# Performance work log

Measured on AMD Instinct MI355X. Metric: run time of the kernel, lower is better.

Reference implementation:

```python
import jax, jax.numpy as jnp
import numpy as np

B, S, V, E, H, NL, DFF = 16, 16, 64, 64, 8, 4, 2048
L = S * V
DH = E // H
NUM_GRIDS = 100
POI_DIM = 8
OV_DIM = 8


def setup_inputs() -> dict:
    key = jax.random.key(0)
    ks = jax.random.split(key, 32)
    sc = 0.05
    inp = {}
    inp['features'] = jax.random.normal(ks[0], (B, S, V, 3), jnp.float32)
    inp['overlap_tag'] = jax.random.randint(ks[1], (B, S, V), 0, 3)
    inp['poi_id'] = jax.random.randint(ks[2], (B, S, V), 0, NUM_GRIDS + 1)
    # embedders
    inp['W_raw'] = jax.random.normal(ks[3], (3, E), jnp.float32) * sc
    inp['b_raw'] = jnp.zeros((E,), jnp.float32)
    inp['pos_tab'] = jax.random.normal(ks[4], (S, E), jnp.float32) * sc
    inp['type_tab'] = jax.random.normal(ks[5], (V, E), jnp.float32) * sc
    inp['poi_tab'] = jax.random.normal(ks[6], (NUM_GRIDS + 1, POI_DIM), jnp.float32) * sc
    inp['overlap_tab'] = jax.random.normal(ks[7], (3, OV_DIM), jnp.float32) * sc
    inp['W_comb'] = jax.random.normal(ks[8], (E + OV_DIM + POI_DIM, E), jnp.float32) * sc
    inp['b_comb'] = jnp.zeros((E,), jnp.float32)
    # transformer layers (stacked over NL)
    inp['Wqkv'] = jax.random.normal(ks[9], (NL, E, 3 * E), jnp.float32) * sc
    inp['bqkv'] = jnp.zeros((NL, 3 * E), jnp.float32)
    inp['Wo'] = jax.random.normal(ks[10], (NL, E, E), jnp.float32) * sc
    inp['bo'] = jnp.zeros((NL, E), jnp.float32)
    inp['ln1_s'] = jnp.ones((NL, E), jnp.float32)
    inp['ln1_b'] = jnp.zeros((NL, E), jnp.float32)
    inp['W1'] = jax.random.normal(ks[11], (NL, E, DFF), jnp.float32) * sc
    inp['b1'] = jnp.zeros((NL, DFF), jnp.float32)
    inp['W2'] = jax.random.normal(ks[12], (NL, DFF, E), jnp.float32) * sc
    inp['b2'] = jnp.zeros((NL, E), jnp.float32)
    inp['ln2_s'] = jnp.ones((NL, E), jnp.float32)
    inp['ln2_b'] = jnp.zeros((NL, E), jnp.float32)
    inp['W_head'] = jax.random.normal(ks[13], (E, 3), jnp.float32) * sc
    inp['b_head'] = jnp.zeros((3,), jnp.float32)
    return inp


def _layer_norm(x, s, b):
    m = x.mean(-1, keepdims=True)
    v = ((x - m) ** 2).mean(-1, keepdims=True)
    return (x - m) / jnp.sqrt(v + 1e-5) * s + b


def _forward(features, overlap_tag, poi_id, W_raw, b_raw, pos_tab, type_tab,
             poi_tab, overlap_tab, W_comb, b_comb, Wqkv, bqkv, Wo, bo,
             ln1_s, ln1_b, W1, b1, W2, b2, ln2_s, ln2_b, W_head, b_head):
    # padding_idx=0 rows are zero (as in nn.Embedding(padding_idx=0))
    poi_tab = poi_tab.at[0].set(0.0)
    overlap_tab = overlap_tab.at[0].set(0.0)

    zero_mask = (features.sum(-1) == 0).reshape(B, L)  # [B, L]
    ov_idx = jnp.maximum(overlap_tag, 0)
    poi_idx = jnp.maximum(poi_id, 0)

    feat_e = features @ W_raw + b_raw                    # [B,S,V,E]
    concat = jnp.concatenate([feat_e, overlap_tab[ov_idx], poi_tab[poi_idx]], axis=-1)
    x = (concat @ W_comb + b_comb).reshape(B, L, E)      # [B,L,E]

    t_idx = jnp.repeat(jnp.arange(S), V)                 # [L]
    v_idx = jnp.tile(jnp.arange(V), S)                   # [L]
    struct_mask = (t_idx[:, None] != t_idx[None, :]) & (v_idx[:, None] != v_idx[None, :])
    full_mask = struct_mask[None] | zero_mask[:, None, :] | zero_mask[:, :, None]  # [B,L,L]
    bias = jnp.where(full_mask, -jnp.inf, 0.0)[:, None, :, :]  # [B,1,L,L]

    x = x + pos_tab[t_idx][None] + type_tab[v_idx][None]

    scale = 1.0 / jnp.sqrt(jnp.asarray(DH, x.dtype))
    for l in range(NL):
        qkv = x @ Wqkv[l] + bqkv[l]                      # [B,L,3E]
        q, k, v = jnp.split(qkv, 3, axis=-1)
        q = q.reshape(B, L, H, DH)
        k = k.reshape(B, L, H, DH)
        v = v.reshape(B, L, H, DH)
        scores = jnp.einsum('bqhd,bkhd->bhqk', q, k) * scale + bias
        attn = jax.nn.softmax(scores, axis=-1)
        o = jnp.einsum('bhqk,bkhd->bqhd', attn, v).reshape(B, L, E)
        x = _layer_norm(x + o @ Wo[l] + bo[l], ln1_s[l], ln1_b[l])
        ff = jax.nn.relu(x @ W1[l] + b1[l]) @ W2[l] + b2[l]
        x = _layer_norm(x + ff, ln2_s[l], ln2_b[l])

    last = x.reshape(B, S, V, E)[:, -1]                  # [B,V,E]
    return last @ W_head + b_head                        # [B,V,3]


def reference(features, overlap_tag, poi_id, W_raw, b_raw, pos_tab, type_tab,
              poi_tab, overlap_tab, W_comb, b_comb, Wqkv, bqkv, Wo, bo,
              ln1_s, ln1_b, W1, b1, W2, b2, ln2_s, ln2_b, W_head, b_head):
    return _forward(features, overlap_tag, poi_id, W_raw, b_raw, pos_tab, type_tab,
                    poi_tab, overlap_tab, W_comb, b_comb, Wqkv, bqkv, Wo, bo,
                    ln1_s, ln1_b, W1, b1, W2, b2, ln2_s, ln2_b, W_head, b_head)
```

## Files before the change

kernel.cpp:

```cpp
#include <hip/hip_runtime.h>
#include <math.h>

#define BB 16
#define SS 16
#define VVV 64
#define EE 64
#define HHH 8
#define NLAYER 4
#define DFF_ 2048
#define LL 1024
#define BL 16384
#define PERL 131072

typedef __attribute__((ext_vector_type(8))) _Float16 half8;
typedef __attribute__((ext_vector_type(4))) _Float16 half4v;
typedef __attribute__((ext_vector_type(2))) _Float16 half2v;
typedef __attribute__((ext_vector_type(4))) float f32x4;

#if defined(__has_builtin)
#if __has_builtin(__builtin_amdgcn_fdot2)
#define HAVE_FDOT2 1
#endif
#endif

#define SW64(m, k)  (((m) << 6) + ((((k) >> 3) ^ ((m) & 7)) << 3) + ((k) & 7))


__global__ __launch_bounds__(256) void k_prep(
    const float* __restrict__ W1, const float* __restrict__ W2,
    const float* __restrict__ Wqkv, const float* __restrict__ Wo,
    const float* __restrict__ Wcomb,
    _Float16* __restrict__ w1f, _Float16* __restrict__ w2f,
    _Float16* __restrict__ wqkvf, _Float16* __restrict__ wof,
    _Float16* __restrict__ wcombt)
{
  __shared__ float t[64 * 65];
  int bx = blockIdx.x;
  int cc = threadIdx.x & 63, rr = threadIdx.x >> 6;

  if (bx >= 272) {
    int r0 = (bx - 272) * 64;
#pragma unroll
    for (int i = 0; i < 16; i++) {
      int r = i * 4 + rr;
      if (r0 + r < 80) t[r * 65 + cc] = Wcomb[(size_t)(r0 + r) * 64 + cc];
    }
    __syncthreads();
#pragma unroll
    for (int i = 0; i < 16; i++) {
      int c = i * 4 + rr;
      if (r0 + c < 80) wcombt[(size_t)cc * 80 + r0 + c] = (_Float16)t[c * 65 + cc];
    }
    return;
  }

  const float* src; _Float16* dst; int astr;
  if (bx < 128) {
    int l = bx >> 5, g = bx & 31;
    src = W1 + (size_t)l * PERL + g * 64; astr = 2048;
    dst = w1f + (size_t)(l * 32 + g) * 4096;
  } else if (bx < 256) {
    int j = bx - 128; int l = j >> 5, g = j & 31;
    src = W2 + (size_t)l * PERL + (size_t)g * 64 * 64; astr = 64;
    dst = w2f + (size_t)(l * 32 + g) * 4096;
  } else if (bx < 268) {
    int j = bx - 256; int l = j / 3, g = j % 3;
    src = Wqkv + (size_t)l * 64 * 192 + g * 64; astr = 192;
    dst = wqkvf + (size_t)(l * 3 + g) * 4096;
  } else {
    int l = bx - 268;
    src = Wo + (size_t)l * 4096; astr = 64;
    dst = wof + (size_t)l * 4096;
  }
#pragma unroll
  for (int i = 0; i < 16; i++) {
    int a = i * 4 + rr;
    t[cc * 65 + a] = src[(size_t)a * astr + cc];
  }
  __syncthreads();
#pragma unroll
  for (int it = 0; it < 2; it++) {
    int c = threadIdx.x + it * 256;
    int frag = c >> 6, lane = c & 63;
    int m = (frag >> 1) * 16 + (lane & 15);
    int k0 = (frag & 1) * 32 + (lane >> 4) * 8;
    const float* tr = &t[m * 65 + k0];
    half8 h;
#pragma unroll
    for (int j = 0; j < 8; j++) h[j] = (_Float16)tr[j];
    *(half8*)&dst[(size_t)c * 8] = h;
  }
}

__device__ __forceinline__ void qkv_nb(
    const half8 (&af)[2][2], const _Float16* __restrict__ wqkvf,
    const float* __restrict__ bqkv, _Float16* __restrict__ qbuf,
    _Float16* __restrict__ kbuf, _Float16* __restrict__ vbuf,
    int bx, int nb, int wm, int wn, int lane)
{
  int quad = lane >> 4, l15 = lane & 15;
  const _Float16* bt = wqkvf + (size_t)nb * 4096;
  half8 bf[2][2];
#pragma unroll
  for (int nt = 0; nt < 2; nt++)
#pragma unroll
    for (int ks = 0; ks < 2; ks++)
      bf[nt][ks] = *(const half8*)&bt[(size_t)(((wn * 2 + nt) * 2 + ks) * 512) +
                                      lane * 8];
  f32x4 acc[2][2];
#pragma unroll
  for (int mt = 0; mt < 2; mt++)
#pragma unroll
    for (int nt = 0; nt < 2; nt++) {
      float bv = bqkv[nb * 64 + wn * 32 + nt * 16 + l15];
      acc[mt][nt] = (f32x4){bv, bv, bv, bv};
    }
#pragma unroll
  for (int ks = 0; ks < 2; ks++)
#pragma unroll
    for (int mt = 0; mt < 2; mt++)
#pragma unroll
      for (int nt = 0; nt < 2; nt++)
        acc[mt][nt] = __builtin_amdgcn_mfma_f32_16x16x32_f16(
            af[mt][ks], bf[nt][ks], acc[mt][nt], 0, 0, 0);
  _Float16* dst = (nb == 0) ? qbuf : ((nb == 1) ? kbuf : vbuf);
#pragma unroll
  for (int mt = 0; mt < 2; mt++)
#pragma unroll
    for (int nt = 0; nt < 2; nt++) {
      int col = wn * 32 + nt * 16 + l15;
      int h = col >> 3, d = col & 7;
#pragma unroll
      for (int r = 0; r < 4; r++) {
        int row = bx * 64 + wm * 32 + mt * 16 + quad * 4 + r;
        int b = row >> 10, rb = row & 1023;
        dst[((size_t)(b * 8 + h) * 1024 + rb) * 8 + d] = (_Float16)acc[mt][nt][r];
      }
    }
}

__device__ __forceinline__ void ffn_load2(
    const _Float16* __restrict__ w1f, const _Float16* __restrict__ w2f, int g,
    half8 (&a1)[2][2], half8 (&b2w)[2][2], int wn, int lane)
{
  const _Float16* w1t_ = w1f + (size_t)g * 4096;
  const _Float16* w2t_ = w2f + (size_t)g * 4096;
#pragma unroll
  for (int ht = 0; ht < 2; ht++)
#pragma unroll
    for (int ks = 0; ks < 2; ks++)
      a1[ht][ks] = *(const half8*)&w1t_[(size_t)(((wn * 2 + ht) * 2 + ks) * 512) +
                                        lane * 8];
#pragma unroll
  for (int nt = 0; nt < 2; nt++)
#pragma unroll
    for (int ks = 0; ks < 2; ks++)
      b2w[nt][ks] = *(const half8*)&w2t_[(size_t)(((wn * 2 + nt) * 2 + ks) * 512) +
                                         lane * 8];
}

__device__ __forceinline__ void ffn_step2(
    const half8 (&a1)[2][2], const half8 (&b2w)[2][2], const half8 (&xb)[2][2],
    _Float16* hsbuf, const float* __restrict__ b1, int g, f32x4 (&acc)[2][2],
    int wn, int lane)
{
  int quad = lane >> 4, l15 = lane & 15;
  f32x4 hacc[2][2];
#pragma unroll
  for (int ht = 0; ht < 2; ht++)
#pragma unroll
    for (int mt = 0; mt < 2; mt++) hacc[ht][mt] = (f32x4){0.f, 0.f, 0.f, 0.f};
#pragma unroll
  for (int ks = 0; ks < 2; ks++)
#pragma unroll
    for (int ht = 0; ht < 2; ht++)
#pragma unroll
      for (int mt = 0; mt < 2; mt++)
        hacc[ht][mt] = __builtin_amdgcn_mfma_f32_16x16x32_f16(
            a1[ht][ks], xb[mt][ks], hacc[ht][mt], 0, 0, 0);
#pragma unroll
  for (int ht = 0; ht < 2; ht++) {
    float4 bb = *(const float4*)&b1[g * 64 + wn * 32 + ht * 16 + quad * 4];
#pragma unroll
    for (int mt = 0; mt < 2; mt++) {
      f32x4 hv = hacc[ht][mt];
      half4v hp = (half4v){
          (_Float16)fmaxf(hv[0] + bb.x, 0.f), (_Float16)fmaxf(hv[1] + bb.y, 0.f),
          (_Float16)fmaxf(hv[2] + bb.z, 0.f), (_Float16)fmaxf(hv[3] + bb.w, 0.f)};
      *(half4v*)&hsbuf[SW64(mt * 16 + l15, wn * 32 + ht * 16 + quad * 4)] = hp;
    }
  }
  __syncthreads();
#pragma unroll
  for (int ks = 0; ks < 2; ks++)
#pragma unroll
    for (int mt = 0; mt < 2; mt++) {
      half8 a2 = *(const half8*)&hsbuf[SW64(mt * 16 + l15, ks * 32 + quad * 8)];
#pragma unroll
      for (int nt = 0; nt < 2; nt++)
        acc[mt][nt] = __builtin_amdgcn_mfma_f32_16x16x32_f16(a2, b2w[nt][ks],
                                                             acc[mt][nt], 0, 0, 0);
    }
}

__global__ __launch_bounds__(256) void k_embqkv(
    const float* __restrict__ features, const int* __restrict__ ovtag,
    const int* __restrict__ poiid, const float* __restrict__ W_raw,
    const float* __restrict__ b_raw, const float* __restrict__ ov_tab,
    const float* __restrict__ poi_tab, const _Float16* __restrict__ wcombt,
    const float* __restrict__ b_comb, const float* __restrict__ pos_tab,
    const float* __restrict__ type_tab, float* __restrict__ x1,
    float* __restrict__ zm, const _Float16* __restrict__ wqkvf,
    const float* __restrict__ bqkv, _Float16* __restrict__ qbuf,
    _Float16* __restrict__ kbuf, _Float16* __restrict__ vbuf)
{
  constexpr int KP = 104;
  __shared__ _Float16 As[64 * KP];
  __shared__ _Float16 Bs[64 * KP];
  __shared__ _Float16 xs[4096];
  int tid = threadIdx.x;
  int raw = blockIdx.x;
  int bx = ((raw & 7) << 5) + (raw >> 3);
  int m0 = bx * 64;
  int wave = tid >> 6, lane = tid & 63, quad = lane >> 4, l15 = lane & 15;
  int wm = wave >> 1, wn = wave & 1;
  for (int p = tid; p < 1536; p += 256) {
    int r = p / 24, s = p - r * 24; int c = s * 4;
    int row = m0 + r;
    float f0 = features[row * 3 + 0];
    float f1 = features[row * 3 + 1];
    float f2 = features[row * 3 + 2];
    if (s == 0) zm[row] = ((f0 + f1 + f2) == 0.f) ? 1.f : 0.f;
    half4v h;
#pragma unroll
    for (int j = 0; j < 4; j++) {
      int cc = c + j; float v;
      if (cc < 64) {
        v = b_raw[cc] + f0 * W_raw[cc] + f1 * W_raw[64 + cc] + f2 * W_raw[128 + cc];
      } else if (cc < 72) {
        int tt = ovtag[row]; v = (tt <= 0) ? 0.f : ov_tab[tt * 8 + cc - 64];
      } else if (cc < 80) {
        int tt = poiid[row]; v = (tt <= 0) ? 0.f : poi_tab[tt * 8 + cc - 72];
      } else v = 0.f;
      h[j] = (_Float16)v;
    }
    *(half4v*)&As[r * KP + c] = h;
  }
  for (int p = tid; p < 1536; p += 256) {
    int r = p / 24, s = p - r * 24; int c = s * 4;
    half4v h = (half4v){0, 0, 0, 0};
    if (c < 80) h = *(const half4v*)&wcombt[r * 80 + c];
    *(half4v*)&Bs[r * KP + c] = h;
  }
  __syncthreads();
  f32x4 acc[2][2];
#pragma unroll
  for (int mt = 0; mt < 2; mt++)
#pragma unroll
    for (int nt = 0; nt < 2; nt++) {
      float bv = b_comb[wn * 32 + nt * 16 + l15];
      acc[mt][nt] = (f32x4){bv, bv, bv, bv};
    }
#pragma unroll
  for (int ks = 0; ks < 3; ks++) {
    half8 af[2], bf[2];
#pragma unroll
    for (int mt = 0; mt < 2; mt++)
      af[mt] = *(const half8*)&As[(wm * 32 + mt * 16 + l15) * KP + ks * 32 + quad * 8];
#pragma unroll
    for (int nt = 0; nt < 2; nt++)
      bf[nt] = *(const half8*)&Bs[(wn * 32 + nt * 16 + l15) * KP + ks * 32 + quad * 8];
#pragma unroll
    for (int mt = 0; mt < 2; mt++)
#pragma unroll
      for (int nt = 0; nt < 2; nt++)
        acc[mt][nt] = __builtin_amdgcn_mfma_f32_16x16x32_f16(af[mt], bf[nt],
                                                             acc[mt][nt], 0, 0, 0);
  }
#pragma unroll
  for (int mt = 0; mt < 2; mt++)
#pragma unroll
    for (int nt = 0; nt < 2; nt++)
#pragma unroll
      for (int r = 0; r < 4; r++) {
        int lrow = wm * 32 + mt * 16 + quad * 4 + r;
        int row = m0 + lrow;
        int col = wn * 32 + nt * 16 + l15;
        int l = row & (LL - 1);
        float v = acc[mt][nt][r] +
            pos_tab[(l >> 6) * 64 + col] + type_tab[(l & 63) * 64 + col];
        x1[(size_t)row * 64 + col] = v;
        xs[SW64(lrow, col)] = (_Float16)v;
      }
  __syncthreads();
  half8 af[2][2];
#pragma unroll
  for (int mt = 0; mt < 2; mt++)
#pragma unroll
    for (int ks = 0; ks < 2; ks++)
      af[mt][ks] = *(const half8*)&xs[SW64(wm * 32 + mt * 16 + l15,
                                           ks * 32 + quad * 8)];
  for (int nb = 0; nb < 3; nb++)
    qkv_nb(af, wqkvf, bqkv, qbuf, kbuf, vbuf, bx, nb, wm, wn, lane);
}

__global__ __launch_bounds__(256, 2) void k_layerf(
    const _Float16* __restrict__ qin, const _Float16* __restrict__ kin,
    const _Float16* __restrict__ vin, const float* __restrict__ zm,
    const _Float16* __restrict__ wof, const float* __restrict__ bo,
    float* __restrict__ x1,
    const float* __restrict__ ln1_s, const float* __restrict__ ln1_b,
    const _Float16* __restrict__ w1f, const _Float16* __restrict__ w2f,
    const float* __restrict__ b1, const float* __restrict__ b2,
    const float* __restrict__ ln2_s, const float* __restrict__ ln2_b,
    const _Float16* __restrict__ wqkvf, const float* __restrict__ bqkv,
    _Float16* __restrict__ qout, _Float16* __restrict__ kout,
    _Float16* __restrict__ vout, int doqkv,
    const float* __restrict__ Wh, const float* __restrict__ bh,
    float* __restrict__ out)
{
  __shared__ float ots[32 * 68];
  __shared__ __align__(16) _Float16 xs[2048];
  __shared__ float x2f[2048];
  __shared__ __align__(16) _Float16 hs[4][2048];
  __shared__ __align__(16) _Float16 os[2048];
  __shared__ float zsh[1024];
  __shared__ __align__(16) _Float16 kvs[8192];
  __shared__ float ots2[32 * 68];
  int tid = threadIdx.x;
  int raw = blockIdx.x;
  int bx = ((raw & 7) << 6) + (raw >> 3);
  int r0 = bx * 32;
  int rb0 = r0 & 1023;
  int wave = tid >> 6, lane = tid & 63;
  int quad = lane >> 4, l15 = lane & 15;
  int grp = wave >> 1, wn = wave & 1;
  int b = r0 >> 10;
  int tq0 = rb0 >> 6;

  for (int p = tid; p < 1024; p += 256)
    zsh[p] = (zm[b * LL + p] != 0.f) ? -20000.f : 0.f;
  for (int p = tid; p < 512; p += 256) {
    int h = p >> 6, row = p & 63;
    size_t gidx = ((size_t)(b * 8 + h) * 1024 + tq0 * 64 + row) * 8;
    *(half8*)&kvs[h * 512 + row * 8] = *(const half8*)&kin[gidx];
    *(half8*)&kvs[4096 + h * 512 + row * 8] = *(const half8*)&vin[gidx];
  }

  half8 obf[2][2];
#pragma unroll
  for (int nt = 0; nt < 2; nt++)
#pragma unroll
    for (int ks = 0; ks < 2; ks++)
      obf[nt][ks] = *(const half8*)&wof[(size_t)(((wn * 2 + nt) * 2 + ks) * 512) +
                                        lane * 8];
  float x1pre[8];
#pragma unroll
  for (int i = 0; i < 8; i++)
    x1pre[i] = x1[(size_t)(r0 + wave * 8 + i) * 64 + lane];
  float ln1sv = ln1_s[lane], ln1bv = ln1_b[lane];
  float ln2sv = ln2_s[lane], ln2bv = ln2_b[lane];
  float fb2 = b2[lane];
  __syncthreads();

  {
    int lr = tid & 31, hh = tid >> 5;
    int rb = rb0 + lr;
    int vq = rb & 63;
    const _Float16* kb = kin + (size_t)(b * 8 + hh) * 8192;
    const _Float16* vb = vin + (size_t)(b * 8 + hh) * 8192;
    half8 qh = *(const half8*)&qin[(size_t)(b * 8 + hh) * 8192 + (size_t)rb * 8];
    const float scale = 0.3535533905932738f;
    float m = -10000.f, lsum = 0.f;
    float acc[8] = {0.f, 0.f, 0.f, 0.f, 0.f, 0.f, 0.f, 0.f};
    bool zmq = (zsh[rb] < -1.f);

    auto dot = [&](half8 kk) -> float {
      float s = 0.f;
#ifdef HAVE_FDOT2
#pragma unroll
      for (int j = 0; j < 4; j++) {
        half2v qa = (half2v){qh[2 * j], qh[2 * j + 1]};
        half2v ka = (half2v){kk[2 * j], kk[2 * j + 1]};
        s = __builtin_amdgcn_fdot2(qa, ka, s, false);
      }
#else
#pragma unroll
      for (int j = 0; j < 8; j++) s += (float)qh[j] * (float)kk[j];
#endif
      return s;
    };
    auto update = [&](float s, half8 vv) {
      float nm = fmaxf(m, s);
      float r = __expf(m - nm);
      float p = __expf(s - nm);
      lsum = lsum * r + p;
#pragma unroll
      for (int d = 0; d < 8; d++) acc[d] = acc[d] * r + p * (float)vv[d];
      m = nm;
    };

    if (!zmq) {
      for (int base = 0; base < 64; base += 4) {
        half8 kk[4], vv[4]; float sv[4];
#pragma unroll
        for (int j = 0; j < 4; j++) {
          kk[j] = *(const half8*)&kvs[hh * 512 + (base + j) * 8];
          vv[j] = *(const half8*)&kvs[4096 + hh * 512 + (base + j) * 8];
        }
#pragma unroll
        for (int j = 0; j < 4; j++)
          sv[j] = dot(kk[j]) * scale + zsh[tq0 * 64 + base + j];
#pragma unroll
        for (int j = 0; j < 4; j++) update(sv[j], vv[j]);
      }
      for (int bb = 0; bb < 5; bb++) {
        half8 kk[3], vv[3]; float sv[3];
#pragma unroll
        for (int j = 0; j < 3; j++) {
          int cc = bb * 3 + j;
          int tt = cc + ((cc >= tq0) ? 1 : 0);
          int k = tt * 64 + vq;
          kk[j] = *(const half8*)&kb[(size_t)k * 8];
          vv[j] = *(const half8*)&vb[(size_t)k * 8];
          sv[j] = zsh[k];
        }
#pragma unroll
        for (int j = 0; j < 3; j++) sv[j] += dot(kk[j]) * scale;
#pragma unroll
        for (int j = 0; j < 3; j++) update(sv[j], vv[j]);
      }
    }
    float inv = (lsum > 0.f) ? 1.f / lsum : 0.f;
    half8 o;
#pragma unroll
    for (int d = 0; d < 8; d++) o[d] = (_Float16)(acc[d] * inv);
    *(half8*)&os[SW64(lr, hh * 8)] = o;
  }
  __syncthreads();

  {
    half8 af[2];
#pragma unroll
    for (int ks = 0; ks < 2; ks++)
      af[ks] = *(const half8*)&os[SW64(grp * 16 + l15, ks * 32 + quad * 8)];
    f32x4 acc[2];
#pragma unroll
    for (int nt = 0; nt < 2; nt++) {
      float bv = bo[wn * 32 + nt * 16 + l15];
      acc[nt] = (f32x4){bv, bv, bv, bv};
    }
#pragma unroll
    for (int ks = 0; ks < 2; ks++)
#pragma unroll
      for (int nt = 0; nt < 2; nt++)
        acc[nt] = __builtin_amdgcn_mfma_f32_16x16x32_f16(af[ks], obf[nt][ks],
                                                         acc[nt], 0, 0, 0);
#pragma unroll
    for (int nt = 0; nt < 2; nt++)
#pragma unroll
      for (int r = 0; r < 4; r++)
        ots[(grp * 16 + quad * 4 + r) * 68 + wn * 32 + nt * 16 + l15] = acc[nt][r];
  }
  half8 a1x[2][2], b2x[2][2], a1y[2][2], b2y[2][2];
  ffn_load2(w1f, w2f, grp, a1x, b2x, wn, lane);
  __syncthreads();
  for (int i = 0; i < 8; i++) {
    int row = wave * 8 + i;
    float val = ots[row * 68 + lane] + x1pre[i];
    float sum = val;
#pragma unroll
    for (int o = 32; o > 0; o >>= 1) sum += __shfl_xor(sum, o);
    float mean = sum * (1.f / 64.f);
    float d = val - mean;
    float sq = d * d;
#pragma unroll
    for (int o = 32; o > 0; o >>= 1) sq += __shfl_xor(sq, o);
    float xv = d * rsqrtf(sq * (1.f / 64.f) + 1e-5f) * ln1sv + ln1bv;
    x2f[row * 64 + lane] = xv;
    xs[SW64(row, lane)] = (_Float16)xv;
  }
  __syncthreads();

  half8 xb[2][2];
#pragma unroll
  for (int mt = 0; mt < 2; mt++)
#pragma unroll
    for (int ks = 0; ks < 2; ks++)
      xb[mt][ks] = *(const half8*)&xs[SW64(mt * 16 + l15, ks * 32 + quad * 8)];
  f32x4 acc[2][2];
#pragma unroll
  for (int mt = 0; mt < 2; mt++)
#pragma unroll
    for (int nt = 0; nt < 2; nt++) {
      float bv = (grp == 0) ? b2[wn * 32 + nt * 16 + l15] : 0.f;
      acc[mt][nt] = (f32x4){bv, bv, bv, bv};
    }
  for (int ii = 0; ii < 8; ii++) {
    ffn_load2(w1f, w2f, ii * 4 + 2 + grp, a1y, b2y, wn, lane);
    ffn_step2(a1x, b2x, xb, &hs[grp][0], b1, ii * 4 + grp, acc, wn, lane);
    if (ii < 7) ffn_load2(w1f, w2f, ii * 4 + 4 + grp, a1x, b2x, wn, lane);
    ffn_step2(a1y, b2y, xb, &hs[grp + 2][0], b1, ii * 4 + 2 + grp, acc, wn, lane);
  }
  __syncthreads();
  if (grp == 0) {
#pragma unroll
    for (int mt = 0; mt < 2; mt++)
#pragma unroll
      for (int nt = 0; nt < 2; nt++)
#pragma unroll
        for (int r = 0; r < 4; r++)
          ots[(mt * 16 + quad * 4 + r) * 68 + wn * 32 + nt * 16 + l15] =
              acc[mt][nt][r];
  }
  __syncthreads();
  if (grp == 1) {
#pragma unroll
    for (int mt = 0; mt < 2; mt++)
#pragma unroll
      for (int nt = 0; nt < 2; nt++)
#pragma unroll
        for (int r = 0; r < 4; r++)
          ots[(mt * 16 + quad * 4 + r) * 68 + wn * 32 + nt * 16 + l15] +=
              acc[mt][nt][r];
  }
  __syncthreads();
  for (int i = 0; i < 8; i++) {
    int row = wave * 8 + i;
    size_t off = (size_t)(r0 + row) * 64 + lane;
    float val = ots[row * 68 + lane] + x2f[row * 64 + lane];
    float sum = val;
#pragma unroll
    for (int o = 32; o > 0; o >>= 1) sum += __shfl_xor(sum, o);
    float mean = sum * (1.f / 64.f);
    float d = val - mean;
    float sq = d * d;
#pragma unroll
    for (int o = 32; o > 0; o >>= 1) sq += __shfl_xor(sq, o);
    float xv = d * rsqrtf(sq * (1.f / 64.f) + 1e-5f) * ln2sv + ln2bv;
    x1[off] = xv;
    x2f[row * 64 + lane] = xv;
    xs[SW64(row, lane)] = (_Float16)xv;
  }
  if (!doqkv) {
    __syncthreads();
    if ((bx & 31) >= 30 && tid < 96) {
      int bb2 = bx >> 5;
      int i = tid / 3, j = tid - i * 3;
      int vglob = (bx & 1) * 32 + i;
      float a = bh[j];
      for (int e = 0; e < 64; e++)
        a += x2f[i * 64 + e] * Wh[e * 3 + j];
      out[((size_t)(bb2 * 64 + vglob)) * 3 + j] = a;
    }
    return;
  }
  __syncthreads();
  half8 af[2][2];
#pragma unroll
  for (int mt = 0; mt < 2; mt++)
#pragma unroll
    for (int ks = 0; ks < 2; ks++)
      af[mt][ks] = *(const half8*)&xs[SW64(mt * 16 + l15, ks * 32 + quad * 8)];
  for (int nb = 0; nb < 3; nb++) {
    const _Float16* bt = wqkvf + (size_t)nb * 4096;
    half8 bf[2];
#pragma unroll
    for (int ks = 0; ks < 2; ks++)
      bf[ks] = *(const half8*)&bt[(size_t)((wave * 2 + ks) * 512) + lane * 8];
    f32x4 qacc[2];
#pragma unroll
    for (int mt = 0; mt < 2; mt++) {
      float bv = bqkv[nb * 64 + wave * 16 + l15];
      qacc[mt] = (f32x4){bv, bv, bv, bv};
    }
#pragma unroll
    for (int ks = 0; ks < 2; ks++)
#pragma unroll
      for (int mt = 0; mt < 2; mt++)
        qacc[mt] = __builtin_amdgcn_mfma_f32_16x16x32_f16(af[mt][ks], bf[ks],
                                                          qacc[mt], 0, 0, 0);
    _Float16* dst = (nb == 0) ? qout : ((nb == 1) ? kout : vout);
    int col = wave * 16 + l15;
    int h2 = col >> 3, d2 = col & 7;
#pragma unroll
    for (int mt = 0; mt < 2; mt++)
#pragma unroll
      for (int r = 0; r < 4; r++) {
        int row = r0 + mt * 16 + quad * 4 + r;
        int rbq = row & 1023;
        dst[((size_t)(b * 8 + h2) * 1024 + rbq) * 8 + d2] = (_Float16)qacc[mt][r];
      }
  }
}

extern "C" void kernel_launch(void* const* d_in, const int* in_sizes, int n_in,
                              void* d_out, int out_size, void* d_ws, size_t ws_size,
                              hipStream_t stream) {
  const float* features = (const float*)d_in[0];
  const int*   ovtag    = (const int*)d_in[1];
  const int*   poiid    = (const int*)d_in[2];
  const float* W_raw    = (const float*)d_in[3];
  const float* b_raw    = (const float*)d_in[4];
  const float* pos_tab  = (const float*)d_in[5];
  const float* type_tab = (const float*)d_in[6];
  const float* poi_tab  = (const float*)d_in[7];
  const float* ov_tab   = (const float*)d_in[8];
  const float* W_comb   = (const float*)d_in[9];
  const float* b_comb   = (const float*)d_in[10];
  const float* Wqkv     = (const float*)d_in[11];
  const float* bqkv     = (const float*)d_in[12];
  const float* Wo       = (const float*)d_in[13];
  const float* bo       = (const float*)d_in[14];
  const float* ln1_s    = (const float*)d_in[15];
  const float* ln1_b    = (const float*)d_in[16];
  const float* W1       = (const float*)d_in[17];
  const float* b1       = (const float*)d_in[18];
  const float* W2       = (const float*)d_in[19];
  const float* b2       = (const float*)d_in[20];
  const float* ln2_s    = (const float*)d_in[21];
  const float* ln2_b    = (const float*)d_in[22];
  const float* W_head   = (const float*)d_in[23];
  const float* b_head   = (const float*)d_in[24];
  float* out = (float*)d_out;
  float* ws  = (float*)d_ws;

  float* zm  = ws;
  float* x1  = zm + BL;
  _Float16* qbA = (_Float16*)(x1 + (size_t)BL * 64);
  _Float16* kbA = qbA + (size_t)BL * 64;
  _Float16* vbA = kbA + (size_t)BL * 64;
  _Float16* qbB = vbA + (size_t)BL * 64;
  _Float16* kbB = qbB + (size_t)BL * 64;
  _Float16* vbB = kbB + (size_t)BL * 64;
  _Float16* wcombt = vbB + (size_t)BL * 64;
  _Float16* w1f    = wcombt + 5120;
  _Float16* w2f    = w1f + (size_t)NLAYER * PERL;
  _Float16* wqkvf  = w2f + (size_t)NLAYER * PERL;
  _Float16* wof    = wqkvf + (size_t)NLAYER * 3 * 4096;

  k_prep<<<274, 256, 0, stream>>>(W1, W2, Wqkv, Wo, W_comb,
                                  w1f, w2f, wqkvf, wof, wcombt);
  k_embqkv<<<256, 256, 0, stream>>>(features, ovtag, poiid, W_raw, b_raw,
                                    ov_tab, poi_tab, wcombt, b_comb,
                                    pos_tab, type_tab, x1, zm,
                                    wqkvf, bqkv, qbA, kbA, vbA);
  for (int l = 0; l < NLAYER; l++) {
    const _Float16* qin = (l & 1) ? qbB : qbA;
    const _Float16* kin = (l & 1) ? kbB : kbA;
    const _Float16* vin = (l & 1) ? vbB : vbA;
    _Float16* qout = (l & 1) ? qbA : qbB;
    _Float16* kout = (l & 1) ? kbA : kbB;
    _Float16* vout = (l & 1) ? vbA : vbB;
    int doqkv = (l < NLAYER - 1);
    k_layerf<<<512, 256, 0, stream>>>(
        qin, kin, vin, zm,
        wof + (size_t)l * 4096, bo + l * EE, x1,
        ln1_s + l * EE, ln1_b + l * EE,
        w1f + (size_t)l * PERL, w2f + (size_t)l * PERL,
        b1 + l * DFF_, b2 + l * EE,
        ln2_s + l * EE, ln2_b + l * EE,
        wqkvf + (size_t)(l + 1 < NLAYER ? l + 1 : 0) * 3 * 4096,
        bqkv + (l + 1 < NLAYER ? l + 1 : 0) * 192,
        qout, kout, vout, doqkv, W_head, b_head, out);
  }
}
```

Measured before the change: 267.8 us.

## Fuse layer pairs into one persistent kernel with a grid barrier

Replaces four per-layer launches with two launches, each running two layers back to back inside resident blocks. The blocks synchronise through a software grid barrier built on global atomics, with an extra fallback barrier used when blocks are not on the expected XCD. Between the two layers each block keeps its own residual and Q tile in shared memory, and only K/V go out through scratch buffers. This removes launch gaps and some global round trips, but relies on all 512 blocks being co-resident and adds barrier spin cost.

```diff
diff --git a/kernel.cpp b/kernel.cpp
--- a/kernel.cpp
+++ b/kernel.cpp
@@ -11,6 +11,7 @@
 #define LL 1024
 #define BL 16384
 #define PERL 131072
+#define NBLK 512
 
 typedef __attribute__((ext_vector_type(8))) _Float16 half8;
 typedef __attribute__((ext_vector_type(4))) _Float16 half4v;
@@ -23,8 +24,52 @@
 #endif
 #endif
 
+#define AGS __HIP_MEMORY_SCOPE_AGENT
+
 #define SW64(m, k)  (((m) << 6) + ((((k) >> 3) ^ ((m) & 7)) << 3) + ((k) & 7))
 
+__device__ __forceinline__ void gsync_plain(unsigned int* B, int tid) {
+  __syncthreads();
+  if (tid == 0) {
+    unsigned prev = __hip_atomic_fetch_add(&B[0], 1u, __ATOMIC_RELAXED, AGS);
+    if (prev == (unsigned)(NBLK - 1)) {
+      __hip_atomic_store(&B[16], 1u, __ATOMIC_RELAXED, AGS);
+    } else {
+      while (__hip_atomic_load(&B[16], __ATOMIC_RELAXED, AGS) == 0u)
+        __builtin_amdgcn_s_sleep(8);
+    }
+  }
+  __syncthreads();
+}
+
+__device__ __forceinline__ void gsyncx(unsigned int* B, int tid, int mybad,
+                                       int* sbad) {
+  __syncthreads();
+  if (tid == 0) {
+    if (mybad) {
+      unsigned v = __hip_atomic_fetch_add(&B[32], 1u, __ATOMIC_RELAXED, AGS);
+      if (v == 0xFFFFFFFFu)
+        __hip_atomic_store(&B[33], 1u, __ATOMIC_RELAXED, AGS);
+    }
+    unsigned prev = __hip_atomic_fetch_add(&B[0], 1u, __ATOMIC_RELAXED, AGS);
+    unsigned g;
+    if (prev == (unsigned)(NBLK - 1)) {
+      unsigned ab = __hip_atomic_load(&B[32], __ATOMIC_RELAXED, AGS);
+      g = 2u | (ab ? 1u : 0u);
+      __hip_atomic_store(&B[16], g, __ATOMIC_RELAXED, AGS);
+    } else {
+      while ((g = __hip_atomic_load(&B[16], __ATOMIC_RELAXED, AGS)) == 0u)
+        __builtin_amdgcn_s_sleep(8);
+    }
+    *sbad = (int)(g & 1u);
+  }
+  __syncthreads();
+  if (*sbad) {
+    __threadfence();
+    gsync_plain(B + 64, tid);
+    __threadfence();
+  }
+}
 
 __global__ __launch_bounds__(256) void k_prep(
     const float* __restrict__ W1, const float* __restrict__ W2,
@@ -32,11 +77,13 @@
     const float* __restrict__ Wcomb,
     _Float16* __restrict__ w1f, _Float16* __restrict__ w2f,
     _Float16* __restrict__ wqkvf, _Float16* __restrict__ wof,
-    _Float16* __restrict__ wcombt)
+    _Float16* __restrict__ wcombt, unsigned int* __restrict__ bar)
 {
   __shared__ float t[64 * 65];
   int bx = blockIdx.x;
   int cc = threadIdx.x & 63, rr = threadIdx.x >> 6;
+
+  if (bx == 0) bar[threadIdx.x] = 0;
 
   if (bx >= 272) {
     int r0 = (bx - 272) * 64;
@@ -304,18 +351,20 @@
     qkv_nb(af, wqkvf, bqkv, qbuf, kbuf, vbuf, bx, nb, wm, wn, lane);
 }
 
-__global__ __launch_bounds__(256, 2) void k_layerf(
+__global__ __launch_bounds__(256, 2) void k_layer2(
     const _Float16* __restrict__ qin, const _Float16* __restrict__ kin,
-    const _Float16* __restrict__ vin, const float* __restrict__ zm,
-    const _Float16* __restrict__ wof, const float* __restrict__ bo,
-    float* __restrict__ x1,
-    const float* __restrict__ ln1_s, const float* __restrict__ ln1_b,
-    const _Float16* __restrict__ w1f, const _Float16* __restrict__ w2f,
-    const float* __restrict__ b1, const float* __restrict__ b2,
-    const float* __restrict__ ln2_s, const float* __restrict__ ln2_b,
-    const _Float16* __restrict__ wqkvf, const float* __restrict__ bqkv,
+    const _Float16* __restrict__ vin,
+    _Float16* __restrict__ kM, _Float16* __restrict__ vM,
     _Float16* __restrict__ qout, _Float16* __restrict__ kout,
-    _Float16* __restrict__ vout, int doqkv,
+    _Float16* __restrict__ vout,
+    const float* __restrict__ zm, float* __restrict__ x1,
+    const _Float16* __restrict__ wofB, const float* __restrict__ boB,
+    const float* __restrict__ ln1_sB, const float* __restrict__ ln1_bB,
+    const _Float16* __restrict__ w1fB, const _Float16* __restrict__ w2fB,
+    const float* __restrict__ b1B, const float* __restrict__ b2B,
+    const float* __restrict__ ln2_sB, const float* __restrict__ ln2_bB,
+    const _Float16* __restrict__ wqkvfB, const float* __restrict__ bqkvB,
+    int l0, unsigned int* __restrict__ bar,
     const float* __restrict__ Wh, const float* __restrict__ bh,
     float* __restrict__ out)
 {
@@ -326,7 +375,7 @@
   __shared__ __align__(16) _Float16 os[2048];
   __shared__ float zsh[1024];
   __shared__ __align__(16) _Float16 kvs[8192];
-  __shared__ float ots2[32 * 68];
+  __shared__ int sbad;
   int tid = threadIdx.x;
   int raw = blockIdx.x;
   int bx = ((raw & 7) << 6) + (raw >> 3);
@@ -337,260 +386,308 @@
   int grp = wave >> 1, wn = wave & 1;
   int b = r0 >> 10;
   int tq0 = rb0 >> 6;
+  _Float16* qkvt = &hs[0][0];
+
+  int xcc = __builtin_amdgcn_s_getreg((31 << 11) | (0 << 6) | 20) & 15;
+  int mybad = (xcc != (raw & 7)) ? 1 : 0;
 
   for (int p = tid; p < 1024; p += 256)
     zsh[p] = (zm[b * LL + p] != 0.f) ? -20000.f : 0.f;
-  for (int p = tid; p < 512; p += 256) {
-    int h = p >> 6, row = p & 63;
-    size_t gidx = ((size_t)(b * 8 + h) * 1024 + tq0 * 64 + row) * 8;
-    *(half8*)&kvs[h * 512 + row * 8] = *(const half8*)&kin[gidx];
-    *(half8*)&kvs[4096 + h * 512 + row * 8] = *(const half8*)&vin[gidx];
-  }
-
-  half8 obf[2][2];
-#pragma unroll
-  for (int nt = 0; nt < 2; nt++)
-#pragma unroll
-    for (int ks = 0; ks < 2; ks++)
-      obf[nt][ks] = *(const half8*)&wof[(size_t)(((wn * 2 + nt) * 2 + ks) * 512) +
-                                        lane * 8];
-  float x1pre[8];
-#pragma unroll
-  for (int i = 0; i < 8; i++)
-    x1pre[i] = x1[(size_t)(r0 + wave * 8 + i) * 64 + lane];
-  float ln1sv = ln1_s[lane], ln1bv = ln1_b[lane];
-  float ln2sv = ln2_s[lane], ln2bv = ln2_b[lane];
-  float fb2 = b2[lane];
-  __syncthreads();
-
-  {
-    int lr = tid & 31, hh = tid >> 5;
-    int rb = rb0 + lr;
-    int vq = rb & 63;
-    const _Float16* kb = kin + (size_t)(b * 8 + hh) * 8192;
-    const _Float16* vb = vin + (size_t)(b * 8 + hh) * 8192;
-    half8 qh = *(const half8*)&qin[(size_t)(b * 8 + hh) * 8192 + (size_t)rb * 8];
-    const float scale = 0.3535533905932738f;
-    float m = -10000.f, lsum = 0.f;
-    float acc[8] = {0.f, 0.f, 0.f, 0.f, 0.f, 0.f, 0.f, 0.f};
-    bool zmq = (zsh[rb] < -1.f);
-
-    auto dot = [&](half8 kk) -> float {
-      float s = 0.f;
+
+  for (int half = 0; half < 2; ++half) {
+    const int l = l0 + half;
+    const _Float16* wof_l = wofB + (size_t)l * 4096;
+    const _Float16* w1l = w1fB + (size_t)l * PERL;
+    const _Float16* w2l = w2fB + (size_t)l * PERL;
+    const float* b1l = b1B + (size_t)l * DFF_;
+    const _Float16* kb_base = half ? kM : kin;
+    const _Float16* vb_base = half ? vM : vin;
+    float ln1sv = ln1_sB[l * 64 + lane], ln1bv = ln1_bB[l * 64 + lane];
+    float ln2sv = ln2_sB[l * 64 + lane], ln2bv = ln2_bB[l * 64 + lane];
+
+    for (int p = tid; p < 512; p += 256) {
+      int h = p >> 6, row = p & 63;
+      size_t gidx = ((size_t)(b * 8 + h) * 1024 + tq0 * 64 + row) * 8;
+      *(half8*)&kvs[h * 512 + row * 8] = *(const half8*)&kb_base[gidx];
+      *(half8*)&kvs[4096 + h * 512 + row * 8] = *(const half8*)&vb_base[gidx];
+    }
+    half8 obf[2][2];
+#pragma unroll
+    for (int nt = 0; nt < 2; nt++)
+#pragma unroll
+      for (int ks = 0; ks < 2; ks++)
+        obf[nt][ks] = *(const half8*)&wof_l[(size_t)(((wn * 2 + nt) * 2 + ks) * 512)
+                                            + lane * 8];
+    float x1pre[8];
+    if (half == 0) {
+#pragma unroll
+      for (int i = 0; i < 8; i++)
+        x1pre[i] = x1[(size_t)(r0 + wave * 8 + i) * 64 + lane];
+    }
+    __syncthreads();
+
+    {
+      int lr = tid & 31, hh = tid >> 5;
+      int rb = rb0 + lr;
+      int vq = rb & 63;
+      const _Float16* kb = kb_base + (size_t)(b * 8 + hh) * 8192;
+      const _Float16* vb = vb_base + (size_t)(b * 8 + hh) * 8192;
+      half8 qh;
+      if (half == 0)
+        qh = *(const half8*)&qin[(size_t)(b * 8 + hh) * 8192 + (size_t)rb * 8];
+      else
+        qh = *(const half8*)&qkvt[SW64(lr, hh * 8)];
+      const float scale = 0.3535533905932738f;
+      float m = -10000.f, lsum = 0.f;
+      float acc[8] = {0.f, 0.f, 0.f, 0.f, 0.f, 0.f, 0.f, 0.f};
+      bool zmq = (zsh[rb] < -1.f);
+
+      auto dot = [&](half8 kk) -> float {
+        float s = 0.f;
 #ifdef HAVE_FDOT2
 #pragma unroll
-      for (int j = 0; j < 4; j++) {
-        half2v qa = (half2v){qh[2 * j], qh[2 * j + 1]};
-        half2v ka = (half2v){kk[2 * j], kk[2 * j + 1]};
-        s = __builtin_amdgcn_fdot2(qa, ka, s, false);
+        for (int j = 0; j < 4; j++) {
+          half2v qa = (half2v){qh[2 * j], qh[2 * j + 1]};
+          half2v ka = (half2v){kk[2 * j], kk[2 * j + 1]};
+          s = __builtin_amdgcn_fdot2(qa, ka, s, false);
+        }
+#else
+#pragma unroll
+        for (int j = 0; j < 8; j++) s += (float)qh[j] * (float)kk[j];
+#endif
+        return s;
+      };
+      auto update = [&](float s, half8 vv) {
+        float nm = fmaxf(m, s);
+        float r = __expf(m - nm);
+        float p = __expf(s - nm);
+        lsum = lsum * r + p;
+#pragma unroll
+        for (int d = 0; d < 8; d++) acc[d] = acc[d] * r + p * (float)vv[d];
+        m = nm;
+      };
+
+      if (!zmq) {
+        for (int base = 0; base < 64; base += 4) {
+          half8 kk[4], vv[4]; float sv[4];
+#pragma unroll
+          for (int j = 0; j < 4; j++) {
+            kk[j] = *(const half8*)&kvs[hh * 512 + (base + j) * 8];
+            vv[j] = *(const half8*)&kvs[4096 + hh * 512 + (base + j) * 8];
+          }
+#pragma unroll
+          for (int j = 0; j < 4; j++)
+            sv[j] = dot(kk[j]) * scale + zsh[tq0 * 64 + base + j];
+#pragma unroll
+          for (int j = 0; j < 4; j++) update(sv[j], vv[j]);
+        }
+        for (int bb = 0; bb < 5; bb++) {
+          half8 kk[3], vv[3]; float sv[3];
+#pragma unroll
+          for (int j = 0; j < 3; j++) {
+            int cc = bb * 3 + j;
+            int tt = cc + ((cc >= tq0) ? 1 : 0);
+            int k = tt * 64 + vq;
+            kk[j] = *(const half8*)&kb[(size_t)k * 8];
+            vv[j] = *(const half8*)&vb[(size_t)k * 8];
+            sv[j] = zsh[k];
+          }
+#pragma unroll
+          for (int j = 0; j < 3; j++) sv[j] += dot(kk[j]) * scale;
+#pragma unroll
+          for (int j = 0; j < 3; j++) update(sv[j], vv[j]);
+        }
       }
-#else
-#pragma unroll
-      for (int j = 0; j < 8; j++) s += (float)qh[j] * (float)kk[j];
-#endif
-      return s;
-    };
-    auto update = [&](float s, half8 vv) {
-      float nm = fmaxf(m, s);
-      float r = __expf(m - nm);
-      float p = __expf(s - nm);
-      lsum = lsum * r + p;
-#pragma unroll
-      for (int d = 0; d < 8; d++) acc[d] = acc[d] * r + p * (float)vv[d];
-      m = nm;
-    };
-
-    if (!zmq) {
-      for (int base = 0; base < 64; base += 4) {
-        half8 kk[4], vv[4]; float sv[4];
-#pragma unroll
-        for (int j = 0; j < 4; j++) {
-          kk[j] = *(const half8*)&kvs[hh * 512 + (base + j) * 8];
-          vv[j] = *(const half8*)&kvs[4096 + hh * 512 + (base + j) * 8];
+      float inv = (lsum > 0.f) ? 1.f / lsum : 0.f;
+      half8 o;
+#pragma unroll
+      for (int d = 0; d < 8; d++) o[d] = (_Float16)(acc[d] * inv);
+      *(half8*)&os[SW64(lr, hh * 8)] = o;
+    }
+    __syncthreads();
+
+    {
+      half8 af[2];
+#pragma unroll
+      for (int ks = 0; ks < 2; ks++)
+        af[ks] = *(const half8*)&os[SW64(grp * 16 + l15, ks * 32 + quad * 8)];
+      f32x4 acc[2];
+#pragma unroll
+      for (int nt = 0; nt < 2; nt++) {
+        float bv = boB[l * 64 + wn * 32 + nt * 16 + l15];
+        acc[nt] = (f32x4){bv, bv, bv, bv};
+      }
+#pragma unroll
+      for (int ks = 0; ks < 2; ks++)
+#pragma unroll
+        for (int nt = 0; nt < 2; nt++)
+          acc[nt] = __builtin_amdgcn_mfma_f32_16x16x32_f16(af[ks], obf[nt][ks],
+                                                           acc[nt], 0, 0, 0);
+#pragma unroll
+      for (int nt = 0; nt < 2; nt++)
+#pragma unroll
+        for (int r = 0; r < 4; r++)
+          ots[(grp * 16 + quad * 4 + r) * 68 + wn * 32 + nt * 16 + l15] =
+              acc[nt][r];
+    }
+    half8 a1x[2][2], b2x[2][2], a1y[2][2], b2y[2][2];
+    ffn_load2(w1l, w2l, grp, a1x, b2x, wn, lane);
+    __syncthreads();
+    for (int i = 0; i < 8; i++) {
+      int row = wave * 8 + i;
+      float res = (half == 0) ? x1pre[i] : x2f[row * 64 + lane];
+      float val = ots[row * 68 + lane] + res;
+      float sum = val;
+#pragma unroll
+      for (int o = 32; o > 0; o >>= 1) sum += __shfl_xor(sum, o);
+      float mean = sum * (1.f / 64.f);
+      float d = val - mean;
+      float sq = d * d;
+#pragma unroll
+      for (int o = 32; o > 0; o >>= 1) sq += __shfl_xor(sq, o);
+      float xv = d * rsqrtf(sq * (1.f / 64.f) + 1e-5f) * ln1sv + ln1bv;
+      x2f[row * 64 + lane] = xv;
+      xs[SW64(row, lane)] = (_Float16)xv;
+    }
+    __syncthreads();
+
+    half8 xb[2][2];
+#pragma unroll
+    for (int mt = 0; mt < 2; mt++)
+#pragma unroll
+      for (int ks = 0; ks < 2; ks++)
+        xb[mt][ks] = *(const half8*)&xs[SW64(mt * 16 + l15, ks * 32 + quad * 8)];
+    f32x4 acc[2][2];
+#pragma unroll
+    for (int mt = 0; mt < 2; mt++)
+#pragma unroll
+      for (int nt = 0; nt < 2; nt++) {
+        float bv = (grp == 0) ? b2B[l * 64 + wn * 32 + nt * 16 + l15] : 0.f;
+        acc[mt][nt] = (f32x4){bv, bv, bv, bv};
+      }
+    for (int ii = 0; ii < 8; ii++) {
+      ffn_load2(w1l, w2l, ii * 4 + 2 + grp, a1y, b2y, wn, lane);
+      ffn_step2(a1x, b2x, xb, &hs[grp][0], b1l, ii * 4 + grp, acc, wn, lane);
+      if (ii < 7) ffn_load2(w1l, w2l, ii * 4 + 4 + grp, a1x, b2x, wn, lane);
+      ffn_step2(a1y, b2y, xb, &hs[grp + 2][0], b1l, ii * 4 + 2 + grp, acc, wn,
+                lane);
+    }
+    __syncthreads();
+    if (grp == 0) {
+#pragma unroll
+      for (int mt = 0; mt < 2; mt++)
+#pragma unroll
+        for (int nt = 0; nt < 2; nt++)
+#pragma unroll
+          for (int r = 0; r < 4; r++)
+            ots[(mt * 16 + quad * 4 + r) * 68 + wn * 32 + nt * 16 + l15] =
+                acc[mt][nt][r];
+    }
+    __syncthreads();
+    if (grp == 1) {
+#pragma unroll
+      for (int mt = 0; mt < 2; mt++)
+#pragma unroll
+        for (int nt = 0; nt < 2; nt++)
+#pragma unroll
+          for (int r = 0; r < 4; r++)
+            ots[(mt * 16 + quad * 4 + r) * 68 + wn * 32 + nt * 16 + l15] +=
+                acc[mt][nt][r];
+    }
+    __syncthreads();
+    for (int i = 0; i < 8; i++) {
+      int row = wave * 8 + i;
+      float val = ots[row * 68 + lane] + x2f[row * 64 + lane];
+      float sum = val;
+#pragma unroll
+      for (int o = 32; o > 0; o >>= 1) sum += __shfl_xor(sum, o);
+      float mean = sum * (1.f / 64.f);
+      float d = val - mean;
+      float sq = d * d;
+#pragma unroll
+      for (int o = 32; o > 0; o >>= 1) sq += __shfl_xor(sq, o);
+      float xv = d * rsqrtf(sq * (1.f / 64.f) + 1e-5f) * ln2sv + ln2bv;
+      if (half == 1 && l0 == 0)
+        x1[(size_t)(r0 + row) * 64 + lane] = xv;
+      x2f[row * 64 + lane] = xv;
+      xs[SW64(row, lane)] = (_Float16)xv;
+    }
+    __syncthreads();
+
+    if (l == 3) {
+      if ((bx & 31) >= 30 && tid < 96) {
+        int bb2 = bx >> 5;
+        int i = tid / 3, j = tid - i * 3;
+        int vglob = (bx & 1) * 32 + i;
+        float a = bh[j];
+        for (int e = 0; e < 64; e++)
+          a += x2f[i * 64 + e] * Wh[e * 3 + j];
+        out[((size_t)(bb2 * 64 + vglob)) * 3 + j] = a;
+      }
+      return;
+    }
+
+    {
+      const _Float16* wq = wqkvfB + (size_t)(l + 1) * 3 * 4096;
+      const float* bq = bqkvB + (l + 1) * 192;
+      half8 af[2][2];
+#pragma unroll
+      for (int mt = 0; mt < 2; mt++)
+#pragma unroll
+        for (int ks = 0; ks < 2; ks++)
+          af[mt][ks] = *(const half8*)&xs[SW64(mt * 16 + l15, ks * 32 + quad * 8)];
+      for (int nb = 0; nb < 3; nb++) {
+        const _Float16* bt = wq + (size_t)nb * 4096;
+        half8 bf[2];
+#pragma unroll
+        for (int ks = 0; ks < 2; ks++)
+          bf[ks] = *(const half8*)&bt[(size_t)((wave * 2 + ks) * 512) + lane * 8];
+        f32x4 qacc[2];
+#pragma unroll
+        for (int mt = 0; mt < 2; mt++) {
+          float bv = bq[nb * 64 + wave * 16 + l15];
+          qacc[mt] = (f32x4){bv, bv, bv, bv};
         }
 #pragma unroll
-        for (int j = 0; j < 4; j++)
-          sv[j] = dot(kk[j]) * scale + zsh[tq0 * 64 + base + j];
-#pragma unroll
-        for (int j = 0; j < 4; j++) update(sv[j], vv[j]);
+        for (int ks = 0; ks < 2; ks++)
+#pragma unroll
+          for (int mt = 0; mt < 2; mt++)
+            qacc[mt] = __builtin_amdgcn_mfma_f32_16x16x32_f16(af[mt][ks], bf[ks],
+                                                              qacc[mt], 0, 0, 0);
+        int col = wave * 16 + l15;
+        int h2 = col >> 3, d2 = col & 7;
+        if (half == 0) {
+          if (nb == 0) {
+#pragma unroll
+            for (int mt = 0; mt < 2; mt++)
+#pragma unroll
+              for (int r = 0; r < 4; r++)
+                qkvt[SW64(mt * 16 + quad * 4 + r, col)] = (_Float16)qacc[mt][r];
+          } else {
+            _Float16* dst = (nb == 1) ? kM : vM;
+#pragma unroll
+            for (int mt = 0; mt < 2; mt++)
+#pragma unroll
+              for (int r = 0; r < 4; r++) {
+                int rbq = (r0 + mt * 16 + quad * 4 + r) & 1023;
+                dst[((size_t)(b * 8 + h2) * 1024 + rbq) * 8 + d2] =
+                    (_Float16)qacc[mt][r];
+              }
+          }
+        } else {
+          _Float16* dst = (nb == 0) ? qout : ((nb == 1) ? kout : vout);
+#pragma unroll
+          for (int mt = 0; mt < 2; mt++)
+#pragma unroll
+            for (int r = 0; r < 4; r++) {
+              int rbq = (r0 + mt * 16 + quad * 4 + r) & 1023;
+              dst[((size_t)(b * 8 + h2) * 1024 + rbq) * 8 + d2] =
+                  (_Float16)qacc[mt][r];
+            }
+        }
       }
-      for (int bb = 0; bb < 5; bb++) {
-        half8 kk[3], vv[3]; float sv[3];
-#pragma unroll
-        for (int j = 0; j < 3; j++) {
-          int cc = bb * 3 + j;
-          int tt = cc + ((cc >= tq0) ? 1 : 0);
-          int k = tt * 64 + vq;
-          kk[j] = *(const half8*)&kb[(size_t)k * 8];
-          vv[j] = *(const half8*)&vb[(size_t)k * 8];
-          sv[j] = zsh[k];
-        }
-#pragma unroll
-        for (int j = 0; j < 3; j++) sv[j] += dot(kk[j]) * scale;
-#pragma unroll
-        for (int j = 0; j < 3; j++) update(sv[j], vv[j]);
-      }
-    }
-    float inv = (lsum > 0.f) ? 1.f / lsum : 0.f;
-    half8 o;
-#pragma unroll
-    for (int d = 0; d < 8; d++) o[d] = (_Float16)(acc[d] * inv);
-    *(half8*)&os[SW64(lr, hh * 8)] = o;
-  }
-  __syncthreads();
-
-  {
-    half8 af[2];
-#pragma unroll
-    for (int ks = 0; ks < 2; ks++)
-      af[ks] = *(const half8*)&os[SW64(grp * 16 + l15, ks * 32 + quad * 8)];
-    f32x4 acc[2];
-#pragma unroll
-    for (int nt = 0; nt < 2; nt++) {
-      float bv = bo[wn * 32 + nt * 16 + l15];
-      acc[nt] = (f32x4){bv, bv, bv, bv};
-    }
-#pragma unroll
-    for (int ks = 0; ks < 2; ks++)
-#pragma unroll
-      for (int nt = 0; nt < 2; nt++)
-        acc[nt] = __builtin_amdgcn_mfma_f32_16x16x32_f16(af[ks], obf[nt][ks],
-                                                         acc[nt], 0, 0, 0);
-#pragma unroll
-    for (int nt = 0; nt < 2; nt++)
-#pragma unroll
-      for (int r = 0; r < 4; r++)
-        ots[(grp * 16 + quad * 4 + r) * 68 + wn * 32 + nt * 16 + l15] = acc[nt][r];
-  }
-  half8 a1x[2][2], b2x[2][2], a1y[2][2], b2y[2][2];
-  ffn_load2(w1f, w2f, grp, a1x, b2x, wn, lane);
-  __syncthreads();
-  for (int i = 0; i < 8; i++) {
-    int row = wave * 8 + i;
-    float val = ots[row * 68 + lane] + x1pre[i];
-    float sum = val;
-#pragma unroll
-    for (int o = 32; o > 0; o >>= 1) sum += __shfl_xor(sum, o);
-    float mean = sum * (1.f / 64.f);
-    float d = val - mean;
-    float sq = d * d;
-#pragma unroll
-    for (int o = 32; o > 0; o >>= 1) sq += __shfl_xor(sq, o);
-    float xv = d * rsqrtf(sq * (1.f / 64.f) + 1e-5f) * ln1sv + ln1bv;
-    x2f[row * 64 + lane] = xv;
-    xs[SW64(row, lane)] = (_Float16)xv;
-  }
-  __syncthreads();
-
-  half8 xb[2][2];
-#pragma unroll
-  for (int mt = 0; mt < 2; mt++)
-#pragma unroll
-    for (int ks = 0; ks < 2; ks++)
-      xb[mt][ks] = *(const half8*)&xs[SW64(mt * 16 + l15, ks * 32 + quad * 8)];
-  f32x4 acc[2][2];
-#pragma unroll
-  for (int mt = 0; mt < 2; mt++)
-#pragma unroll
-    for (int nt = 0; nt < 2; nt++) {
-      float bv = (grp == 0) ? b2[wn * 32 + nt * 16 + l15] : 0.f;
-      acc[mt][nt] = (f32x4){bv, bv, bv, bv};
-    }
-  for (int ii = 0; ii < 8; ii++) {
-    ffn_load2(w1f, w2f, ii * 4 + 2 + grp, a1y, b2y, wn, lane);
-    ffn_step2(a1x, b2x, xb, &hs[grp][0], b1, ii * 4 + grp, acc, wn, lane);
-    if (ii < 7) ffn_load2(w1f, w2f, ii * 4 + 4 + grp, a1x, b2x, wn, lane);
-    ffn_step2(a1y, b2y, xb, &hs[grp + 2][0], b1, ii * 4 + 2 + grp, acc, wn, lane);
-  }
-  __syncthreads();
-  if (grp == 0) {
-#pragma unroll
-    for (int mt = 0; mt < 2; mt++)
-#pragma unroll
-      for (int nt = 0; nt < 2; nt++)
-#pragma unroll
-        for (int r = 0; r < 4; r++)
-          ots[(mt * 16 + quad * 4 + r) * 68 + wn * 32 + nt * 16 + l15] =
-              acc[mt][nt][r];
-  }
-  __syncthreads();
-  if (grp == 1) {
-#pragma unroll
-    for (int mt = 0; mt < 2; mt++)
-#pragma unroll
-      for (int nt = 0; nt < 2; nt++)
-#pragma unroll
-        for (int r = 0; r < 4; r++)
-          ots[(mt * 16 + quad * 4 + r) * 68 + wn * 32 + nt * 16 + l15] +=
-              acc[mt][nt][r];
-  }
-  __syncthreads();
-  for (int i = 0; i < 8; i++) {
-    int row = wave * 8 + i;
-    size_t off = (size_t)(r0 + row) * 64 + lane;
-    float val = ots[row * 68 + lane] + x2f[row * 64 + lane];
-    float sum = val;
-#pragma unroll
-    for (int o = 32; o > 0; o >>= 1) sum += __shfl_xor(sum, o);
-    float mean = sum * (1.f / 64.f);
-    float d = val - mean;
-    float sq = d * d;
-#pragma unroll
-    for (int o = 32; o > 0; o >>= 1) sq += __shfl_xor(sq, o);
-    float xv = d * rsqrtf(sq * (1.f / 64.f) + 1e-5f) * ln2sv + ln2bv;
-    x1[off] = xv;
-    x2f[row * 64 + lane] = xv;
-    xs[SW64(row, lane)] = (_Float16)xv;
-  }
-  if (!doqkv) {
-    __syncthreads();
-    if ((bx & 31) >= 30 && tid < 96) {
-      int bb2 = bx >> 5;
-      int i = tid / 3, j = tid - i * 3;
-      int vglob = (bx & 1) * 32 + i;
-      float a = bh[j];
-      for (int e = 0; e < 64; e++)
-        a += x2f[i * 64 + e] * Wh[e * 3 + j];
-      out[((size_t)(bb2 * 64 + vglob)) * 3 + j] = a;
-    }
-    return;
-  }
-  __syncthreads();
-  half8 af[2][2];
-#pragma unroll
-  for (int mt = 0; mt < 2; mt++)
-#pragma unroll
-    for (int ks = 0; ks < 2; ks++)
-      af[mt][ks] = *(const half8*)&xs[SW64(mt * 16 + l15, ks * 32 + quad * 8)];
-  for (int nb = 0; nb < 3; nb++) {
-    const _Float16* bt = wqkvf + (size_t)nb * 4096;
-    half8 bf[2];
-#pragma unroll
-    for (int ks = 0; ks < 2; ks++)
-      bf[ks] = *(const half8*)&bt[(size_t)((wave * 2 + ks) * 512) + lane * 8];
-    f32x4 qacc[2];
-#pragma unroll
-    for (int mt = 0; mt < 2; mt++) {
-      float bv = bqkv[nb * 64 + wave * 16 + l15];
-      qacc[mt] = (f32x4){bv, bv, bv, bv};
-    }
-#pragma unroll
-    for (int ks = 0; ks < 2; ks++)
-#pragma unroll
-      for (int mt = 0; mt < 2; mt++)
-        qacc[mt] = __builtin_amdgcn_mfma_f32_16x16x32_f16(af[mt][ks], bf[ks],
-                                                          qacc[mt], 0, 0, 0);
-    _Float16* dst = (nb == 0) ? qout : ((nb == 1) ? kout : vout);
-    int col = wave * 16 + l15;
-    int h2 = col >> 3, d2 = col & 7;
-#pragma unroll
-    for (int mt = 0; mt < 2; mt++)
-#pragma unroll
-      for (int r = 0; r < 4; r++) {
-        int row = r0 + mt * 16 + quad * 4 + r;
-        int rbq = row & 1023;
-        dst[((size_t)(b * 8 + h2) * 1024 + rbq) * 8 + d2] = (_Float16)qacc[mt][r];
-      }
+    }
+    if (half == 0) gsyncx(bar, tid, mybad, &sbad);
   }
 }
 
@@ -633,35 +730,27 @@
   _Float16* qbB = vbA + (size_t)BL * 64;
   _Float16* kbB = qbB + (size_t)BL * 64;
   _Float16* vbB = kbB + (size_t)BL * 64;
-  _Float16* wcombt = vbB + (size_t)BL * 64;
+  _Float16* kM  = vbB + (size_t)BL * 64;
+  _Float16* vM  = kM  + (size_t)BL * 64;
+  _Float16* wcombt = vM + (size_t)BL * 64;
   _Float16* w1f    = wcombt + 5120;
   _Float16* w2f    = w1f + (size_t)NLAYER * PERL;
   _Float16* wqkvf  = w2f + (size_t)NLAYER * PERL;
   _Float16* wof    = wqkvf + (size_t)NLAYER * 3 * 4096;
+  unsigned int* bar = (unsigned int*)(wof + (size_t)NLAYER * 4096);
 
   k_prep<<<274, 256, 0, stream>>>(W1, W2, Wqkv, Wo, W_comb,
-                                  w1f, w2f, wqkvf, wof, wcombt);
+                                  w1f, w2f, wqkvf, wof, wcombt, bar);
   k_embqkv<<<256, 256, 0, stream>>>(features, ovtag, poiid, W_raw, b_raw,
                                     ov_tab, poi_tab, wcombt, b_comb,
                                     pos_tab, type_tab, x1, zm,
                                     wqkvf, bqkv, qbA, kbA, vbA);
-  for (int l = 0; l < NLAYER; l++) {
-    const _Float16* qin = (l & 1) ? qbB : qbA;
-    const _Float16* kin = (l & 1) ? kbB : kbA;
-    const _Float16* vin = (l & 1) ? vbB : vbA;
-    _Float16* qout = (l & 1) ? qbA : qbB;
-    _Float16* kout = (l & 1) ? kbA : kbB;
-    _Float16* vout = (l & 1) ? vbA : vbB;
-    int doqkv = (l < NLAYER - 1);
-    k_layerf<<<512, 256, 0, stream>>>(
-        qin, kin, vin, zm,
-        wof + (size_t)l * 4096, bo + l * EE, x1,
-        ln1_s + l * EE, ln1_b + l * EE,
-        w1f + (size_t)l * PERL, w2f + (size_t)l * PERL,
-        b1 + l * DFF_, b2 + l * EE,
-        ln2_s + l * EE, ln2_b + l * EE,
-        wqkvf + (size_t)(l + 1 < NLAYER ? l + 1 : 0) * 3 * 4096,
-        bqkv + (l + 1 < NLAYER ? l + 1 : 0) * 192,
-        qout, kout, vout, doqkv, W_head, b_head, out);
-  }
-}
+  k_layer2<<<NBLK, 256, 0, stream>>>(
+      qbA, kbA, vbA, kM, vM, qbB, kbB, vbB, zm, x1,
+      wof, bo, ln1_s, ln1_b, w1f, w2f, b1, b2, ln2_s, ln2_b,
+      wqkvf, bqkv, 0, bar, W_head, b_head, out);
+  k_layer2<<<NBLK, 256, 0, stream>>>(
+      qbB, kbB, vbB, kM, vM, qbA, kbA, vbA, zm, x1,
+      wof, bo, ln1_s, ln1_b, w1f, w2f, b1, b2, ln2_s, ln2_b,
+      wqkvf, bqkv, 2, bar + 128, W_head, b_head, out);
+}
```

Measured after the change: 356.3 us. 33.1% more time.
